# Performance work log

Hardware: AMD Instinct MI355X
Metric: run time of the kernel (lower is better)

The kernel has to match this reference:

```python
import jax, jax.numpy as jnp
from jax import lax
import numpy as np


def setup_inputs() -> dict:
    key = jax.random.key(0)
    kx, = jax.random.split(key, 1)
    B, T = 4096, 4096
    x = jax.random.normal(kx, (B, T), dtype=jnp.float32)
    omega_log = jnp.asarray(0.0, dtype=jnp.float32)
    alpha_log = jnp.asarray(0.0, dtype=jnp.float32)
    beta_log = jnp.asarray(0.0, dtype=jnp.float32)
    return {"x": x, "omega_log": omega_log, "alpha_log": alpha_log, "beta_log": beta_log}


def reference(x, omega_log, alpha_log, beta_log):
    # x: [B, T]
    ea = jnp.exp(alpha_log)
    eb = jnp.exp(beta_log)
    denom = 1.0 + ea + eb
    omega = jnp.exp(omega_log)
    alpha = ea / denom
    beta = eb / denom

    # initial variance: unbiased sample variance over time (torch.var default ddof=1)
    s0 = jnp.var(x, axis=1, ddof=1)  # [B]

    xsq = jnp.swapaxes(x[:, :-1] ** 2, 0, 1)  # [T-1, B]

    def step(s_prev, x2_t):
        s_t = omega + alpha * x2_t + beta * s_prev
        return s_t, s_t

    _, rest = lax.scan(step, s0, xsq)  # rest: [T-1, B]
    sigma2 = jnp.concatenate([s0[None, :], rest], axis=0)  # [T, B]
    return jnp.sqrt(jnp.swapaxes(sigma2, 0, 1))  # [B, T]
```

## Files before the change

kernel.cpp:

```cpp
#include <hip/hip_runtime.h>
#include <math.h>

#define B_ROWS 4096
#define T_COLS 4096
#define NTHREADS 1024
#define CHUNK 4
#define NWAVES (NTHREADS / 64)

__device__ __forceinline__ float rfl(float v) {
    return __int_as_float(__builtin_amdgcn_readfirstlane(__float_as_int(v)));
}

__global__ __launch_bounds__(NTHREADS, 8) void garch_fused(
    const float* __restrict__ x,
    const float* __restrict__ p_omega_log,
    const float* __restrict__ p_alpha_log,
    const float* __restrict__ p_beta_log,
    float* __restrict__ out)
{
    __shared__ float wA[NWAVES], wB[NWAVES], rSum[NWAVES], rSsq[NWAVES];

    const int t    = threadIdx.x;
    const int lane = t & 63;
    const int wv   = t >> 6;
    const long rbase = (long)blockIdx.x * T_COLS;

    float4 v = reinterpret_cast<const float4*>(x + rbase)[t];

    float prevg = 0.0f;
    if (lane == 0 && t > 0) prevg = x[rbase + 4 * t - 1];

    float ea_p  = expf(p_alpha_log[0]);
    float eb_p  = expf(p_beta_log[0]);
    float denom = 1.0f + ea_p + eb_p;
    float omega = rfl(expf(p_omega_log[0]));
    float alpha = rfl(ea_p / denom);
    float beta  = rfl(eb_p / denom);
    float beta2 = beta * beta;
    float beta3 = beta2 * beta;
    float beta4 = beta2 * beta2;

    float x0 = v.x, x1 = v.y, x2 = v.z, x3 = v.w;

    float prev = __shfl_up(x3, 1);
    if (lane == 0) prev = prevg;

    float sum = ((x0 + x1) + (x2 + x3));
    float ssq = x0 * x0;
    ssq = fmaf(x1, x1, ssq);
    ssq = fmaf(x2, x2, ssq);
    ssq = fmaf(x3, x3, ssq);

    float z = (t > 0) ? fmaf(alpha, prev * prev, omega) : 0.0f;
    z = fmaf(beta, z, fmaf(alpha, x0 * x0, omega));
    z = fmaf(beta, z, fmaf(alpha, x1 * x1, omega));
    z = fmaf(beta, z, fmaf(alpha, x2 * x2, omega));
    float bpart = z;
    float apart = (t == 0) ? beta3 : beta4;

    float s1 = sum, s2 = ssq;
#pragma unroll
    for (int d = 32; d > 0; d >>= 1) {
        s1 += __shfl_xor(s1, d);
        s2 += __shfl_xor(s2, d);
    }

    float ia = apart, ib = bpart;
#pragma unroll
    for (int d = 1; d < 64; d <<= 1) {
        float pa = __shfl_up(ia, d);
        float pb = __shfl_up(ib, d);
        if (lane >= d) { ib = fmaf(ia, pb, ib); ia = ia * pa; }
    }

    if (lane == 0)  { rSum[wv] = s1; rSsq[wv] = s2; }
    if (lane == 63) { wA[wv] = ia;   wB[wv] = ib;  }
    __syncthreads();

    float tsum = 0.0f, tssq = 0.0f;
#pragma unroll
    for (int w = 0; w < NWAVES; ++w) { tsum += rSum[w]; tssq += rSsq[w]; }
    float s0 = (tssq - tsum * tsum * (1.0f / T_COLS)) * (1.0f / (T_COLS - 1));
    s0 = fmaxf(s0, 0.0f);

    float sw = s0;
#pragma unroll
    for (int w = 0; w < NWAVES - 1; ++w)
        if (w < wv) sw = fmaf(wA[w], sw, wB[w]);

    float pea = __shfl_up(ia, 1);
    float peb = __shfl_up(ib, 1);
    if (lane == 0) { pea = 1.0f; peb = 0.0f; }
    float s = fmaf(pea, sw, peb);

    float4 q;
    if (t == 0) {
        q.x = __builtin_amdgcn_sqrtf(s);
        float zz = s;
        zz = fmaf(beta, zz, fmaf(alpha, x0 * x0, omega)); q.y = __builtin_amdgcn_sqrtf(zz);
        zz = fmaf(beta, zz, fmaf(alpha, x1 * x1, omega)); q.z = __builtin_amdgcn_sqrtf(zz);
        zz = fmaf(beta, zz, fmaf(alpha, x2 * x2, omega)); q.w = __builtin_amdgcn_sqrtf(zz);
    } else {
        float zz = s;
        zz = fmaf(beta, zz, fmaf(alpha, prev * prev, omega)); q.x = __builtin_amdgcn_sqrtf(zz);
        zz = fmaf(beta, zz, fmaf(alpha, x0 * x0, omega));     q.y = __builtin_amdgcn_sqrtf(zz);
        zz = fmaf(beta, zz, fmaf(alpha, x1 * x1, omega));     q.z = __builtin_amdgcn_sqrtf(zz);
        zz = fmaf(beta, zz, fmaf(alpha, x2 * x2, omega));     q.w = __builtin_amdgcn_sqrtf(zz);
    }

    reinterpret_cast<float4*>(out + rbase)[t] = q;
}

extern "C" void kernel_launch(void* const* d_in, const int* in_sizes, int n_in,
                              void* d_out, int out_size, void* d_ws, size_t ws_size,
                              hipStream_t stream) {
    const float* x         = (const float*)d_in[0];
    const float* omega_log = (const float*)d_in[1];
    const float* alpha_log = (const float*)d_in[2];
    const float* beta_log  = (const float*)d_in[3];
    float* out = (float*)d_out;

    garch_fused<<<B_ROWS, NTHREADS, 0, stream>>>(x, omega_log, alpha_log, beta_log, out);
}
```

Before: 127.1 us.

## Process eight rows per block with next-row prefetch and double-buffered LDS

Each block now handles eight consecutive rows instead of one, and the grid shrinks accordingly. The float4 load for the next row is issued before the current row is computed, so global load latency can overlap with the scan and reduction work. Per-wave partials go into double-buffered shared arrays, which allows a single lightweight barrier (lgkmcnt wait plus s_barrier) per row, and the cross-wave sums are read back as float4. This cuts per-block launch overhead and hides latency, at the cost of fewer resident blocks and serialized rows within each block.

```diff
diff --git a/kernel.cpp b/kernel.cpp
--- a/kernel.cpp
+++ b/kernel.cpp
@@ -4,11 +4,17 @@
 #define B_ROWS 4096
 #define T_COLS 4096
 #define NTHREADS 1024
-#define CHUNK 4
 #define NWAVES (NTHREADS / 64)
+#define RPB 8
+#define NBLOCKS (B_ROWS / RPB)
 
 __device__ __forceinline__ float rfl(float v) {
     return __int_as_float(__builtin_amdgcn_readfirstlane(__float_as_int(v)));
+}
+
+__device__ __forceinline__ void lds_barrier() {
+    asm volatile("s_waitcnt lgkmcnt(0)" ::: "memory");
+    __builtin_amdgcn_s_barrier();
 }
 
 __global__ __launch_bounds__(NTHREADS, 8) void garch_fused(
@@ -18,17 +24,17 @@
     const float* __restrict__ p_beta_log,
     float* __restrict__ out)
 {
-    __shared__ float wA[NWAVES], wB[NWAVES], rSum[NWAVES], rSsq[NWAVES];
+    __shared__ float wA[2][NWAVES], wB[2][NWAVES];
+    __shared__ float rSum[2][NWAVES], rSsq[2][NWAVES];
 
     const int t    = threadIdx.x;
     const int lane = t & 63;
     const int wv   = t >> 6;
-    const long rbase = (long)blockIdx.x * T_COLS;
+    const long row0 = (long)blockIdx.x * RPB;
 
-    float4 v = reinterpret_cast<const float4*>(x + rbase)[t];
-
-    float prevg = 0.0f;
-    if (lane == 0 && t > 0) prevg = x[rbase + 4 * t - 1];
+    float4 vc = reinterpret_cast<const float4*>(x + row0 * T_COLS)[t];
+    float pg = 0.0f;
+    if (lane == 0 && t > 0) pg = x[row0 * T_COLS + 4 * t - 1];
 
     float ea_p  = expf(p_alpha_log[0]);
     float eb_p  = expf(p_beta_log[0]);
@@ -36,79 +42,96 @@
     float omega = rfl(expf(p_omega_log[0]));
     float alpha = rfl(ea_p / denom);
     float beta  = rfl(eb_p / denom);
-    float beta2 = beta * beta;
-    float beta3 = beta2 * beta;
-    float beta4 = beta2 * beta2;
+    float beta3 = beta * beta * beta;
+    float beta4 = beta3 * beta;
 
-    float x0 = v.x, x1 = v.y, x2 = v.z, x3 = v.w;
+#pragma unroll
+    for (int g = 0; g < RPB; ++g) {
+        const long row = row0 + g;
 
-    float prev = __shfl_up(x3, 1);
-    if (lane == 0) prev = prevg;
+        float4 vn = make_float4(0.0f, 0.0f, 0.0f, 0.0f);
+        float pgn = 0.0f;
+        if (g + 1 < RPB) {
+            vn = reinterpret_cast<const float4*>(x + (row + 1) * T_COLS)[t];
+            if (lane == 0 && t > 0) pgn = x[(row + 1) * T_COLS + 4 * t - 1];
+        }
 
-    float sum = ((x0 + x1) + (x2 + x3));
-    float ssq = x0 * x0;
-    ssq = fmaf(x1, x1, ssq);
-    ssq = fmaf(x2, x2, ssq);
-    ssq = fmaf(x3, x3, ssq);
+        float x0 = vc.x, x1 = vc.y, x2 = vc.z, x3 = vc.w;
 
-    float z = (t > 0) ? fmaf(alpha, prev * prev, omega) : 0.0f;
-    z = fmaf(beta, z, fmaf(alpha, x0 * x0, omega));
-    z = fmaf(beta, z, fmaf(alpha, x1 * x1, omega));
-    z = fmaf(beta, z, fmaf(alpha, x2 * x2, omega));
-    float bpart = z;
-    float apart = (t == 0) ? beta3 : beta4;
+        float prev = __shfl_up(x3, 1);
+        if (lane == 0) prev = pg;
 
-    float s1 = sum, s2 = ssq;
+        float s1 = (x0 + x1) + (x2 + x3);
+        float s2 = x0 * x0;
+        s2 = fmaf(x1, x1, s2);
+        s2 = fmaf(x2, x2, s2);
+        s2 = fmaf(x3, x3, s2);
+
+        float z = (t > 0) ? fmaf(alpha, prev * prev, omega) : 0.0f;
+        z = fmaf(beta, z, fmaf(alpha, x0 * x0, omega));
+        z = fmaf(beta, z, fmaf(alpha, x1 * x1, omega));
+        z = fmaf(beta, z, fmaf(alpha, x2 * x2, omega));
+        float ib = z;
+        float ia = (t == 0) ? beta3 : beta4;
+
 #pragma unroll
-    for (int d = 32; d > 0; d >>= 1) {
-        s1 += __shfl_xor(s1, d);
-        s2 += __shfl_xor(s2, d);
+        for (int d = 32; d > 0; d >>= 1) {
+            s1 += __shfl_xor(s1, d);
+            s2 += __shfl_xor(s2, d);
+        }
+
+#pragma unroll
+        for (int d = 1; d < 64; d <<= 1) {
+            float pa = __shfl_up(ia, d);
+            float pb = __shfl_up(ib, d);
+            if (lane >= d) { ib = fmaf(ia, pb, ib); ia = ia * pa; }
+        }
+
+        if (lane == 0)  { rSum[g & 1][wv] = s1; rSsq[g & 1][wv] = s2; }
+        if (lane == 63) { wA[g & 1][wv] = ia;   wB[g & 1][wv] = ib;  }
+
+        lds_barrier();
+
+        float tsum = 0.0f, tssq = 0.0f;
+#pragma unroll
+        for (int w4 = 0; w4 < NWAVES / 4; ++w4) {
+            float4 a = *reinterpret_cast<const float4*>(&rSum[g & 1][4 * w4]);
+            float4 b = *reinterpret_cast<const float4*>(&rSsq[g & 1][4 * w4]);
+            tsum += (a.x + a.y) + (a.z + a.w);
+            tssq += (b.x + b.y) + (b.z + b.w);
+        }
+        float s0 = (tssq - tsum * tsum * (1.0f / T_COLS)) * (1.0f / (T_COLS - 1));
+        s0 = fmaxf(s0, 0.0f);
+
+        float sw = s0;
+#pragma unroll
+        for (int w = 0; w < NWAVES - 1; ++w)
+            if (w < wv) sw = fmaf(wA[g & 1][w], sw, wB[g & 1][w]);
+
+        float pea = __shfl_up(ia, 1);
+        float peb = __shfl_up(ib, 1);
+        if (lane == 0) { pea = 1.0f; peb = 0.0f; }
+        float s = fmaf(pea, sw, peb);
+
+        float4 q;
+        if (t == 0) {
+            q.x = __builtin_amdgcn_sqrtf(s);
+            float zz = s;
+            zz = fmaf(beta, zz, fmaf(alpha, x0 * x0, omega)); q.y = __builtin_amdgcn_sqrtf(zz);
+            zz = fmaf(beta, zz, fmaf(alpha, x1 * x1, omega)); q.z = __builtin_amdgcn_sqrtf(zz);
+            zz = fmaf(beta, zz, fmaf(alpha, x2 * x2, omega)); q.w = __builtin_amdgcn_sqrtf(zz);
+        } else {
+            float zz = s;
+            zz = fmaf(beta, zz, fmaf(alpha, prev * prev, omega)); q.x = __builtin_amdgcn_sqrtf(zz);
+            zz = fmaf(beta, zz, fmaf(alpha, x0 * x0, omega));     q.y = __builtin_amdgcn_sqrtf(zz);
+            zz = fmaf(beta, zz, fmaf(alpha, x1 * x1, omega));     q.z = __builtin_amdgcn_sqrtf(zz);
+            zz = fmaf(beta, zz, fmaf(alpha, x2 * x2, omega));     q.w = __builtin_amdgcn_sqrtf(zz);
+        }
+
+        reinterpret_cast<float4*>(out + row * T_COLS)[t] = q;
+
+        vc = vn; pg = pgn;
     }
-
-    float ia = apart, ib = bpart;
-#pragma unroll
-    for (int d = 1; d < 64; d <<= 1) {
-        float pa = __shfl_up(ia, d);
-        float pb = __shfl_up(ib, d);
-        if (lane >= d) { ib = fmaf(ia, pb, ib); ia = ia * pa; }
-    }
-
-    if (lane == 0)  { rSum[wv] = s1; rSsq[wv] = s2; }
-    if (lane == 63) { wA[wv] = ia;   wB[wv] = ib;  }
-    __syncthreads();
-
-    float tsum = 0.0f, tssq = 0.0f;
-#pragma unroll
-    for (int w = 0; w < NWAVES; ++w) { tsum += rSum[w]; tssq += rSsq[w]; }
-    float s0 = (tssq - tsum * tsum * (1.0f / T_COLS)) * (1.0f / (T_COLS - 1));
-    s0 = fmaxf(s0, 0.0f);
-
-    float sw = s0;
-#pragma unroll
-    for (int w = 0; w < NWAVES - 1; ++w)
-        if (w < wv) sw = fmaf(wA[w], sw, wB[w]);
-
-    float pea = __shfl_up(ia, 1);
-    float peb = __shfl_up(ib, 1);
-    if (lane == 0) { pea = 1.0f; peb = 0.0f; }
-    float s = fmaf(pea, sw, peb);
-
-    float4 q;
-    if (t == 0) {
-        q.x = __builtin_amdgcn_sqrtf(s);
-        float zz = s;
-        zz = fmaf(beta, zz, fmaf(alpha, x0 * x0, omega)); q.y = __builtin_amdgcn_sqrtf(zz);
-        zz = fmaf(beta, zz, fmaf(alpha, x1 * x1, omega)); q.z = __builtin_amdgcn_sqrtf(zz);
-        zz = fmaf(beta, zz, fmaf(alpha, x2 * x2, omega)); q.w = __builtin_amdgcn_sqrtf(zz);
-    } else {
-        float zz = s;
-        zz = fmaf(beta, zz, fmaf(alpha, prev * prev, omega)); q.x = __builtin_amdgcn_sqrtf(zz);
-        zz = fmaf(beta, zz, fmaf(alpha, x0 * x0, omega));     q.y = __builtin_amdgcn_sqrtf(zz);
-        zz = fmaf(beta, zz, fmaf(alpha, x1 * x1, omega));     q.z = __builtin_amdgcn_sqrtf(zz);
-        zz = fmaf(beta, zz, fmaf(alpha, x2 * x2, omega));     q.w = __builtin_amdgcn_sqrtf(zz);
-    }
-
-    reinterpret_cast<float4*>(out + rbase)[t] = q;
 }
 
 extern "C" void kernel_launch(void* const* d_in, const int* in_sizes, int n_in,
@@ -120,5 +143,5 @@
     const float* beta_log  = (const float*)d_in[3];
     float* out = (float*)d_out;
 
-    garch_fused<<<B_ROWS, NTHREADS, 0, stream>>>(x, omega_log, alpha_log, beta_log, out);
+    garch_fused<<<NBLOCKS, NTHREADS, 0, stream>>>(x, omega_log, alpha_log, beta_log, out);
 }
```

After: 128.0 us. Within noise of the previous version (+0.8%).

## Process one row per wavefront with 64 elements per lane

Applied to the files above, without the earlier changes.

Moves from one 1024-thread block per row to one wavefront per row, with each lane holding 64 contiguous elements in registers. The cross-wave LDS reduction and __syncthreads are gone: the variance reduction and the linear-recurrence scan now use only intra-wave shuffles. Each lane splits its sequential recurrence into two independent 31/32-step halves to shorten the dependency chain. The cost is heavy register use (64 floats per lane plus temporaries), which may lower occupancy. Each lane also reads and writes 256 contiguous bytes, so adjacent lanes touch addresses 256 bytes apart and global accesses are no longer coalesced across lanes.

```diff
diff --git a/kernel.cpp b/kernel.cpp
--- a/kernel.cpp
+++ b/kernel.cpp
@@ -3,32 +3,33 @@
 
 #define B_ROWS 4096
 #define T_COLS 4096
-#define NTHREADS 1024
-#define CHUNK 4
-#define NWAVES (NTHREADS / 64)
+#define NTHREADS 256
+#define WPB (NTHREADS / 64)
+#define NBLOCKS (B_ROWS / WPB)
 
 __device__ __forceinline__ float rfl(float v) {
     return __int_as_float(__builtin_amdgcn_readfirstlane(__float_as_int(v)));
 }
 
-__global__ __launch_bounds__(NTHREADS, 8) void garch_fused(
+#define STEP(z, xv) fmaf(beta, (z), fmaf(alpha, (xv) * (xv), omega))
+#define SQ(z) __builtin_amdgcn_sqrtf(z)
+
+__global__ __launch_bounds__(NTHREADS, 4) void garch_fused(
     const float* __restrict__ x,
     const float* __restrict__ p_omega_log,
     const float* __restrict__ p_alpha_log,
     const float* __restrict__ p_beta_log,
     float* __restrict__ out)
 {
-    __shared__ float wA[NWAVES], wB[NWAVES], rSum[NWAVES], rSsq[NWAVES];
+    const int lane = threadIdx.x & 63;
+    const int wv   = threadIdx.x >> 6;
+    const long row = (long)blockIdx.x * WPB + wv;
 
-    const int t    = threadIdx.x;
-    const int lane = t & 63;
-    const int wv   = t >> 6;
-    const long rbase = (long)blockIdx.x * T_COLS;
-
-    float4 v = reinterpret_cast<const float4*>(x + rbase)[t];
-
-    float prevg = 0.0f;
-    if (lane == 0 && t > 0) prevg = x[rbase + 4 * t - 1];
+    const float4* xr4 = reinterpret_cast<const float4*>(x + row * T_COLS) + lane * 16;
+    float xs[64];
+#pragma unroll
+    for (int j = 0; j < 16; ++j)
+        *reinterpret_cast<float4*>(&xs[4 * j]) = xr4[j];
 
     float ea_p  = expf(p_alpha_log[0]);
     float eb_p  = expf(p_beta_log[0]);
@@ -36,36 +37,46 @@
     float omega = rfl(expf(p_omega_log[0]));
     float alpha = rfl(ea_p / denom);
     float beta  = rfl(eb_p / denom);
-    float beta2 = beta * beta;
-    float beta3 = beta2 * beta;
-    float beta4 = beta2 * beta2;
+    float beta2  = beta * beta;
+    float beta4  = beta2 * beta2;
+    float beta8  = beta4 * beta4;
+    float beta16 = beta8 * beta8;
+    float beta32 = beta16 * beta16;
+    float beta31 = beta16 * beta8 * beta4 * beta2 * beta;
 
-    float x0 = v.x, x1 = v.y, x2 = v.z, x3 = v.w;
+    float a0 = 0, a1 = 0, a2 = 0, a3 = 0, q0 = 0, q1 = 0, q2 = 0, q3 = 0;
+#pragma unroll
+    for (int k = 0; k < 64; k += 4) {
+        a0 += xs[k + 0]; q0 = fmaf(xs[k + 0], xs[k + 0], q0);
+        a1 += xs[k + 1]; q1 = fmaf(xs[k + 1], xs[k + 1], q1);
+        a2 += xs[k + 2]; q2 = fmaf(xs[k + 2], xs[k + 2], q2);
+        a3 += xs[k + 3]; q3 = fmaf(xs[k + 3], xs[k + 3], q3);
+    }
+    float s1 = (a0 + a1) + (a2 + a3);
+    float s2 = (q0 + q1) + (q2 + q3);
 
-    float prev = __shfl_up(x3, 1);
-    if (lane == 0) prev = prevg;
+    float prev = __shfl_up(xs[63], 1);
 
-    float sum = ((x0 + x1) + (x2 + x3));
-    float ssq = x0 * x0;
-    ssq = fmaf(x1, x1, ssq);
-    ssq = fmaf(x2, x2, ssq);
-    ssq = fmaf(x3, x3, ssq);
+    float zA = (lane > 0) ? fmaf(alpha, prev * prev, omega) : 0.0f;
+    float zB = 0.0f;
+#pragma unroll
+    for (int k = 0; k < 31; ++k) {
+        zA = STEP(zA, xs[k]);
+        zB = STEP(zB, xs[k + 31]);
+    }
+    zB = STEP(zB, xs[62]);
+    float aA = (lane == 0) ? beta31 : beta32;
+    float ib = fmaf(beta32, zA, zB);
+    float ia = aA * beta32;
 
-    float z = (t > 0) ? fmaf(alpha, prev * prev, omega) : 0.0f;
-    z = fmaf(beta, z, fmaf(alpha, x0 * x0, omega));
-    z = fmaf(beta, z, fmaf(alpha, x1 * x1, omega));
-    z = fmaf(beta, z, fmaf(alpha, x2 * x2, omega));
-    float bpart = z;
-    float apart = (t == 0) ? beta3 : beta4;
-
-    float s1 = sum, s2 = ssq;
 #pragma unroll
     for (int d = 32; d > 0; d >>= 1) {
         s1 += __shfl_xor(s1, d);
         s2 += __shfl_xor(s2, d);
     }
+    float s0 = (s2 - s1 * s1 * (1.0f / T_COLS)) * (1.0f / (T_COLS - 1));
+    s0 = fmaxf(s0, 0.0f);
 
-    float ia = apart, ib = bpart;
 #pragma unroll
     for (int d = 1; d < 64; d <<= 1) {
         float pa = __shfl_up(ia, d);
@@ -73,42 +84,45 @@
         if (lane >= d) { ib = fmaf(ia, pb, ib); ia = ia * pa; }
     }
 
-    if (lane == 0)  { rSum[wv] = s1; rSsq[wv] = s2; }
-    if (lane == 63) { wA[wv] = ia;   wB[wv] = ib;  }
-    __syncthreads();
-
-    float tsum = 0.0f, tssq = 0.0f;
-#pragma unroll
-    for (int w = 0; w < NWAVES; ++w) { tsum += rSum[w]; tssq += rSsq[w]; }
-    float s0 = (tssq - tsum * tsum * (1.0f / T_COLS)) * (1.0f / (T_COLS - 1));
-    s0 = fmaxf(s0, 0.0f);
-
-    float sw = s0;
-#pragma unroll
-    for (int w = 0; w < NWAVES - 1; ++w)
-        if (w < wv) sw = fmaf(wA[w], sw, wB[w]);
-
     float pea = __shfl_up(ia, 1);
     float peb = __shfl_up(ib, 1);
     if (lane == 0) { pea = 1.0f; peb = 0.0f; }
-    float s = fmaf(pea, sw, peb);
+    float eA = fmaf(pea, s0, peb);
+    float eB = fmaf(aA, eA, zA);
 
-    float4 q;
-    if (t == 0) {
-        q.x = __builtin_amdgcn_sqrtf(s);
-        float zz = s;
-        zz = fmaf(beta, zz, fmaf(alpha, x0 * x0, omega)); q.y = __builtin_amdgcn_sqrtf(zz);
-        zz = fmaf(beta, zz, fmaf(alpha, x1 * x1, omega)); q.z = __builtin_amdgcn_sqrtf(zz);
-        zz = fmaf(beta, zz, fmaf(alpha, x2 * x2, omega)); q.w = __builtin_amdgcn_sqrtf(zz);
-    } else {
-        float zz = s;
-        zz = fmaf(beta, zz, fmaf(alpha, prev * prev, omega)); q.x = __builtin_amdgcn_sqrtf(zz);
-        zz = fmaf(beta, zz, fmaf(alpha, x0 * x0, omega));     q.y = __builtin_amdgcn_sqrtf(zz);
-        zz = fmaf(beta, zz, fmaf(alpha, x1 * x1, omega));     q.z = __builtin_amdgcn_sqrtf(zz);
-        zz = fmaf(beta, zz, fmaf(alpha, x2 * x2, omega));     q.w = __builtin_amdgcn_sqrtf(zz);
+    float4* orow4 = reinterpret_cast<float4*>(out + row * T_COLS) + lane * 16;
+
+    {
+        float z;
+        float4 q;
+        if (lane == 0) { z = eA; }
+        else           { z = fmaf(beta, eA, fmaf(alpha, prev * prev, omega)); }
+        q.x = SQ(z);
+        z = STEP(z, xs[0]); q.y = SQ(z);
+        z = STEP(z, xs[1]); q.z = SQ(z);
+        z = STEP(z, xs[2]); q.w = SQ(z);
+        orow4[0] = q;
+#pragma unroll
+        for (int j = 1; j < 8; ++j) {
+            z = STEP(z, xs[4 * j - 1]); q.x = SQ(z);
+            z = STEP(z, xs[4 * j + 0]); q.y = SQ(z);
+            z = STEP(z, xs[4 * j + 1]); q.z = SQ(z);
+            z = STEP(z, xs[4 * j + 2]); q.w = SQ(z);
+            orow4[j] = q;
+        }
     }
-
-    reinterpret_cast<float4*>(out + rbase)[t] = q;
+    {
+        float z = eB;
+        float4 q;
+#pragma unroll
+        for (int j = 8; j < 16; ++j) {
+            z = STEP(z, xs[4 * j - 1]); q.x = SQ(z);
+            z = STEP(z, xs[4 * j + 0]); q.y = SQ(z);
+            z = STEP(z, xs[4 * j + 1]); q.z = SQ(z);
+            z = STEP(z, xs[4 * j + 2]); q.w = SQ(z);
+            orow4[j] = q;
+        }
+    }
 }
 
 extern "C" void kernel_launch(void* const* d_in, const int* in_sizes, int n_in,
@@ -120,5 +134,5 @@
     const float* beta_log  = (const float*)d_in[3];
     float* out = (float*)d_out;
 
-    garch_fused<<<B_ROWS, NTHREADS, 0, stream>>>(x, omega_log, alpha_log, beta_log, out);
+    garch_fused<<<NBLOCKS, NTHREADS, 0, stream>>>(x, omega_log, alpha_log, beta_log, out);
 }
```

Result: no change. 129.4 us (+1.8%).

## Process each row with one wavefront, striping the scan across sixteen chunks

Applied to the files above, without the earlier changes.

Instead of one 1024-thread block per row with a shared-memory cross-wave scan and a block barrier, each 64-lane wavefront now handles a whole row. It computes the variance reduction in a first pass, then runs sixteen sequential wave-level affine scans with a carried state and prefetches the next stripe. This removes LDS traffic and __syncthreads. In exchange the row is read twice and each wave carries a long serial chain of shuffles, which could cost latency.

```diff
diff --git a/kernel.cpp b/kernel.cpp
--- a/kernel.cpp
+++ b/kernel.cpp
@@ -3,32 +3,31 @@
 
 #define B_ROWS 4096
 #define T_COLS 4096
-#define NTHREADS 1024
-#define CHUNK 4
-#define NWAVES (NTHREADS / 64)
+#define NTHREADS 256
+#define WPB 4
+#define NBLOCKS (B_ROWS / WPB)
+#define NSTRIPE 16
 
 __device__ __forceinline__ float rfl(float v) {
     return __int_as_float(__builtin_amdgcn_readfirstlane(__float_as_int(v)));
 }
 
-__global__ __launch_bounds__(NTHREADS, 8) void garch_fused(
+#define STEP(z, xv) fmaf(beta, (z), fmaf(alpha, (xv) * (xv), omega))
+#define SQ(z) __builtin_amdgcn_sqrtf(z)
+
+__global__ __launch_bounds__(NTHREADS, 4) void garch_fused(
     const float* __restrict__ x,
     const float* __restrict__ p_omega_log,
     const float* __restrict__ p_alpha_log,
     const float* __restrict__ p_beta_log,
     float* __restrict__ out)
 {
-    __shared__ float wA[NWAVES], wB[NWAVES], rSum[NWAVES], rSsq[NWAVES];
+    const int lane = threadIdx.x & 63;
+    const int wv   = threadIdx.x >> 6;
+    const long row = (long)blockIdx.x * WPB + wv;
 
-    const int t    = threadIdx.x;
-    const int lane = t & 63;
-    const int wv   = t >> 6;
-    const long rbase = (long)blockIdx.x * T_COLS;
-
-    float4 v = reinterpret_cast<const float4*>(x + rbase)[t];
-
-    float prevg = 0.0f;
-    if (lane == 0 && t > 0) prevg = x[rbase + 4 * t - 1];
+    const float4* X4 = reinterpret_cast<const float4*>(x + row * T_COLS);
+    float4*       O4 = reinterpret_cast<float4*>(out + row * T_COLS);
 
     float ea_p  = expf(p_alpha_log[0]);
     float eb_p  = expf(p_beta_log[0]);
@@ -40,75 +39,72 @@
     float beta3 = beta2 * beta;
     float beta4 = beta2 * beta2;
 
-    float x0 = v.x, x1 = v.y, x2 = v.z, x3 = v.w;
-
-    float prev = __shfl_up(x3, 1);
-    if (lane == 0) prev = prevg;
-
-    float sum = ((x0 + x1) + (x2 + x3));
-    float ssq = x0 * x0;
-    ssq = fmaf(x1, x1, ssq);
-    ssq = fmaf(x2, x2, ssq);
-    ssq = fmaf(x3, x3, ssq);
-
-    float z = (t > 0) ? fmaf(alpha, prev * prev, omega) : 0.0f;
-    z = fmaf(beta, z, fmaf(alpha, x0 * x0, omega));
-    z = fmaf(beta, z, fmaf(alpha, x1 * x1, omega));
-    z = fmaf(beta, z, fmaf(alpha, x2 * x2, omega));
-    float bpart = z;
-    float apart = (t == 0) ? beta3 : beta4;
-
-    float s1 = sum, s2 = ssq;
+    float sum = 0.0f, ssq = 0.0f;
+#pragma unroll
+    for (int s = 0; s < NSTRIPE; ++s) {
+        float4 a = X4[64 * s + lane];
+        sum += (a.x + a.y) + (a.z + a.w);
+        ssq = fmaf(a.x, a.x, ssq); ssq = fmaf(a.y, a.y, ssq);
+        ssq = fmaf(a.z, a.z, ssq); ssq = fmaf(a.w, a.w, ssq);
+    }
 #pragma unroll
     for (int d = 32; d > 0; d >>= 1) {
-        s1 += __shfl_xor(s1, d);
-        s2 += __shfl_xor(s2, d);
+        sum += __shfl_xor(sum, d);
+        ssq += __shfl_xor(ssq, d);
     }
-
-    float ia = apart, ib = bpart;
-#pragma unroll
-    for (int d = 1; d < 64; d <<= 1) {
-        float pa = __shfl_up(ia, d);
-        float pb = __shfl_up(ib, d);
-        if (lane >= d) { ib = fmaf(ia, pb, ib); ia = ia * pa; }
-    }
-
-    if (lane == 0)  { rSum[wv] = s1; rSsq[wv] = s2; }
-    if (lane == 63) { wA[wv] = ia;   wB[wv] = ib;  }
-    __syncthreads();
-
-    float tsum = 0.0f, tssq = 0.0f;
-#pragma unroll
-    for (int w = 0; w < NWAVES; ++w) { tsum += rSum[w]; tssq += rSsq[w]; }
-    float s0 = (tssq - tsum * tsum * (1.0f / T_COLS)) * (1.0f / (T_COLS - 1));
+    float s0 = (ssq - sum * sum * (1.0f / T_COLS)) * (1.0f / (T_COLS - 1));
     s0 = fmaxf(s0, 0.0f);
 
-    float sw = s0;
+    float E = s0;
+    float carryX = 0.0f;
+    float4 a = X4[lane];
 #pragma unroll
-    for (int w = 0; w < NWAVES - 1; ++w)
-        if (w < wv) sw = fmaf(wA[w], sw, wB[w]);
+    for (int s = 0; s < NSTRIPE; ++s) {
+        float4 an = a;
+        if (s + 1 < NSTRIPE) an = X4[64 * (s + 1) + lane];
 
-    float pea = __shfl_up(ia, 1);
-    float peb = __shfl_up(ib, 1);
-    if (lane == 0) { pea = 1.0f; peb = 0.0f; }
-    float s = fmaf(pea, sw, peb);
+        float xm1 = __shfl_up(a.w, 1);
+        if (lane == 0) xm1 = carryX;
 
-    float4 q;
-    if (t == 0) {
-        q.x = __builtin_amdgcn_sqrtf(s);
-        float zz = s;
-        zz = fmaf(beta, zz, fmaf(alpha, x0 * x0, omega)); q.y = __builtin_amdgcn_sqrtf(zz);
-        zz = fmaf(beta, zz, fmaf(alpha, x1 * x1, omega)); q.z = __builtin_amdgcn_sqrtf(zz);
-        zz = fmaf(beta, zz, fmaf(alpha, x2 * x2, omega)); q.w = __builtin_amdgcn_sqrtf(zz);
-    } else {
-        float zz = s;
-        zz = fmaf(beta, zz, fmaf(alpha, prev * prev, omega)); q.x = __builtin_amdgcn_sqrtf(zz);
-        zz = fmaf(beta, zz, fmaf(alpha, x0 * x0, omega));     q.y = __builtin_amdgcn_sqrtf(zz);
-        zz = fmaf(beta, zz, fmaf(alpha, x1 * x1, omega));     q.z = __builtin_amdgcn_sqrtf(zz);
-        zz = fmaf(beta, zz, fmaf(alpha, x2 * x2, omega));     q.w = __builtin_amdgcn_sqrtf(zz);
+        float ia, ib;
+        if (s == 0 && lane == 0) {
+            float zb = fmaf(alpha, a.x * a.x, omega);
+            zb = STEP(zb, a.y); zb = STEP(zb, a.z);
+            ia = beta3; ib = zb;
+        } else {
+            float zb = fmaf(alpha, xm1 * xm1, omega);
+            zb = STEP(zb, a.x); zb = STEP(zb, a.y); zb = STEP(zb, a.z);
+            ia = beta4; ib = zb;
+        }
+
+#pragma unroll
+        for (int d = 1; d < 64; d <<= 1) {
+            float pa = __shfl_up(ia, d);
+            float pb = __shfl_up(ib, d);
+            if (lane >= d) { ib = fmaf(ia, pb, ib); ia = ia * pa; }
+        }
+
+        float pea = __shfl_up(ia, 1);
+        float peb = __shfl_up(ib, 1);
+        if (lane == 0) { pea = 1.0f; peb = 0.0f; }
+        float e = fmaf(pea, E, peb);
+
+        float4 q;
+        float z;
+        if (s == 0 && lane == 0) { z = e; }
+        else                     { z = STEP(e, xm1); }
+        q.x = SQ(z);
+        z = STEP(z, a.x); q.y = SQ(z);
+        z = STEP(z, a.y); q.z = SQ(z);
+        z = STEP(z, a.z); q.w = SQ(z);
+        O4[64 * s + lane] = q;
+
+        float ia63 = __shfl(ia, 63);
+        float ib63 = __shfl(ib, 63);
+        E = fmaf(ia63, E, ib63);
+        carryX = __shfl(a.w, 63);
+        a = an;
     }
-
-    reinterpret_cast<float4*>(out + rbase)[t] = q;
 }
 
 extern "C" void kernel_launch(void* const* d_in, const int* in_sizes, int n_in,
@@ -120,5 +116,5 @@
     const float* beta_log  = (const float*)d_in[3];
     float* out = (float*)d_out;
 
-    garch_fused<<<B_ROWS, NTHREADS, 0, stream>>>(x, omega_log, alpha_log, beta_log, out);
+    garch_fused<<<NBLOCKS, NTHREADS, 0, stream>>>(x, omega_log, alpha_log, beta_log, out);
 }
```

New measurement: 121.6 us. 1.05x faster.
